# Optimization experiments

Hardware: AMD Instinct MI355X
Metric: run time of the kernel (lower is better)

Reference implementation:

```python
import jax, jax.numpy as jnp
import numpy as np

BATCH = 2048
TEMP = 0.5
EPS = 1e-12  # matches F.normalize default eps


def setup_inputs() -> dict:
    key = jax.random.key(0)
    k1, k2 = jax.random.split(key)
    emb_i = jax.random.normal(k1, (BATCH, 256), dtype=jnp.float32)
    emb_j = jax.random.normal(k2, (BATCH, 256), dtype=jnp.float32)
    return {"emb_i": emb_i, "emb_j": emb_j}


def _l2_normalize(x):
    norm = jnp.sqrt(jnp.sum(x * x, axis=1, keepdims=True))
    return x / jnp.maximum(norm, EPS)


def reference(emb_i, emb_j):
    n = emb_i.shape[0]  # = BATCH
    z_i = _l2_normalize(emb_i)
    z_j = _l2_normalize(emb_j)
    z = jnp.concatenate([z_i, z_j], axis=0)            # [2N, D]
    # cosine similarity of normalized vectors == plain GEMM
    sim = jnp.einsum('id,jd->ij', z, z)                # [2N, 2N]
    # positive pairs: diag offsets +N and -N
    sim_i_j = jnp.diagonal(sim, offset=n)              # [N]
    sim_j_i = jnp.diagonal(sim, offset=-n)             # [N]
    positives = jnp.concatenate([sim_i_j, sim_j_i])    # [2N]
    neg_mask = 1.0 - jnp.eye(2 * n, dtype=sim.dtype)   # [2N, 2N]
    numerator = jnp.exp(positives / TEMP)
    denominator = jnp.sum(neg_mask * jnp.exp(sim / TEMP), axis=1)  # [2N]
    loss_partial = -jnp.log(numerator / denominator)
    return jnp.sum(loss_partial) / (2 * n)
```

## Files before the change

### kernel.cpp

```cpp
#include <hip/hip_runtime.h>
#include <hip/hip_bf16.h>
#include <math.h>

#define NB        2048
#define TWO_N     4096
#define DIM       256
#define EPS       1e-12f
#define NT1D      (TWO_N / 128)
#define NTILES    (NT1D * (NT1D + 1) / 2)


typedef __attribute__((ext_vector_type(8))) short  bf16x8;
typedef __attribute__((ext_vector_type(4))) float  f32x4;

__global__ __launch_bounds__(256) void nrm_kernel(
    const float* __restrict__ emb_i, const float* __restrict__ emb_j,
    short* __restrict__ zt, float* __restrict__ pos,
    float* __restrict__ out)
{
    int t = threadIdx.x;
    int wave = t >> 6, lane = t & 63;
    int r = blockIdx.x * 4 + wave;
    float4 a = ((const float4*)(emb_i + (size_t)r * DIM))[lane];
    float4 b = ((const float4*)(emb_j + (size_t)r * DIM))[lane];
    float sa = a.x*a.x + a.y*a.y + a.z*a.z + a.w*a.w;
    float sb = b.x*b.x + b.y*b.y + b.z*b.z + b.w*b.w;
    float sd = a.x*b.x + a.y*b.y + a.z*b.z + a.w*b.w;
    #pragma unroll
    for (int off = 32; off >= 1; off >>= 1) {
        sa += __shfl_xor(sa, off, 64);
        sb += __shfl_xor(sb, off, 64);
        sd += __shfl_xor(sd, off, 64);
    }
    float si = 1.0f / fmaxf(sqrtf(sa), EPS);
    float sj = 1.0f / fmaxf(sqrtf(sb), EPS);

    int dst = (r >> 4) * 4096 + (lane >> 3) * 512 + ((lane >> 1) & 3) * 128
            + (r & 15) * 8 + (lane & 1) * 4;

    union { __hip_bfloat16 h[4]; uint2 u; } pk;
    pk.h[0] = __float2bfloat16(a.x * si);
    pk.h[1] = __float2bfloat16(a.y * si);
    pk.h[2] = __float2bfloat16(a.z * si);
    pk.h[3] = __float2bfloat16(a.w * si);
    *(uint2*)(zt + dst) = pk.u;
    pk.h[0] = __float2bfloat16(b.x * sj);
    pk.h[1] = __float2bfloat16(b.y * sj);
    pk.h[2] = __float2bfloat16(b.z * sj);
    pk.h[3] = __float2bfloat16(b.w * sj);
    *(uint2*)(zt + dst + 128 * 4096) = pk.u;

    if (lane == 0) pos[r] = sd * si * sj;
    if (blockIdx.x == 0 && t == 0) out[0] = 0.0f;
}

#define MFMA1(Av, Bv, m, n) \
    acc[m][n] = __builtin_amdgcn_mfma_f32_16x16x32_bf16(Av, Bv, acc[m][n], 0, 0, 0);

#define MFMA_ROW(Av, B0v, B1v, B2v, B3v, m) \
    MFMA1(Av, B0v, m, 0) MFMA1(Av, B1v, m, 1) \
    MFMA1(Av, B2v, m, 2) MFMA1(Av, B3v, m, 3)

#define MMSTEP(A0v, A1v, A2v, A3v, B0v, B1v, B2v, B3v) \
    MFMA_ROW(A0v, B0v, B1v, B2v, B3v, 0) \
    MFMA_ROW(A1v, B0v, B1v, B2v, B3v, 1) \
    MFMA_ROW(A2v, B0v, B1v, B2v, B3v, 2) \
    MFMA_ROW(A3v, B0v, B1v, B2v, B3v, 3)

#define SB __builtin_amdgcn_sched_barrier(0);

#define BAR \
    SB \
    asm volatile("s_waitcnt lgkmcnt(0)" ::: "memory"); \
    SB \
    __builtin_amdgcn_s_barrier(); \
    SB

#define SLDX(X, c) \
    G##X##0 = *(const bf16x8*)(stg_base + 0 * 4096 + (c) * 512); \
    G##X##1 = *(const bf16x8*)(stg_base + 1 * 4096 + (c) * 512); \
    G##X##2 = *(const bf16x8*)(stg_base + 2 * 4096 + (c) * 512); \
    G##X##3 = *(const bf16x8*)(stg_base + 3 * 4096 + (c) * 512);

#define DSWX(X, bs) \
    *(bf16x8*)&lds[(bs)*8192 + (p0+0)*512 + l8] = G##X##0; \
    *(bf16x8*)&lds[(bs)*8192 + (p0+1)*512 + l8] = G##X##1; \
    *(bf16x8*)&lds[(bs)*8192 + (p0+2)*512 + l8] = G##X##2; \
    *(bf16x8*)&lds[(bs)*8192 + (p0+3)*512 + l8] = G##X##3;

#define COMPUTE(bs) \
    { \
        bf16x8 fa0 = *(const bf16x8*)&lds[(bs)*8192 + (wm4+0)*512 + l8]; \
        bf16x8 fa1 = *(const bf16x8*)&lds[(bs)*8192 + (wm4+1)*512 + l8]; \
        bf16x8 fa2 = *(const bf16x8*)&lds[(bs)*8192 + (wm4+2)*512 + l8]; \
        bf16x8 fa3 = *(const bf16x8*)&lds[(bs)*8192 + (wm4+3)*512 + l8]; \
        bf16x8 fb0 = *(const bf16x8*)&lds[(bs)*8192 + 4096 + (wn4+0)*512 + l8]; \
        bf16x8 fb1 = *(const bf16x8*)&lds[(bs)*8192 + 4096 + (wn4+1)*512 + l8]; \
        bf16x8 fb2 = *(const bf16x8*)&lds[(bs)*8192 + 4096 + (wn4+2)*512 + l8]; \
        bf16x8 fb3 = *(const bf16x8*)&lds[(bs)*8192 + 4096 + (wn4+3)*512 + l8]; \
        MMSTEP(fa0, fa1, fa2, fa3, fb0, fb1, fb2, fb3) \
    }

__global__ __launch_bounds__(256, 3) void simexp_kernel(
    const short* __restrict__ zt, float* __restrict__ part)
{
    __shared__ short lds[2 * 8192];

    int id = blockIdx.x;
    int by = (int)((sqrtf(8.0f * (float)id + 1.0f) - 1.0f) * 0.5f);
    while ((by + 1) * (by + 2) / 2 <= id) ++by;
    while (by * (by + 1) / 2 > id) --by;
    int bx = id - by * (by + 1) / 2;

    int t = threadIdx.x;
    int w = t >> 6, lane = t & 63;
    int quad = lane >> 4, c16 = lane & 15;
    int wm = w >> 1, wn = w & 1;
    int wm4 = wm * 4, wn4 = wn * 4;
    int l8 = lane * 8;
    int p0 = w * 4;
    int rbase = bx * 128 + wm * 64;
    int jbase = by * 128 + wn * 64;

    const short* stg_base = zt
        + (size_t)((w < 2 ? bx : by) * 8 + (w & 1) * 4) * 4096 + l8;

    f32x4 acc[4][4];
    #pragma unroll
    for (int mt = 0; mt < 4; ++mt)
        #pragma unroll
        for (int nt = 0; nt < 4; ++nt)
            acc[mt][nt] = (f32x4){0.f, 0.f, 0.f, 0.f};

    bf16x8 GA0, GA1, GA2, GA3;
    bf16x8 GB0, GB1, GB2, GB3;

    SLDX(A, 0)
    DSWX(A, 0)
    SLDX(B, 1)
    BAR
    SLDX(A, 2) SB
    COMPUTE(0) SB
    DSWX(B, 1)
    BAR
    DSWX(A, 0) SB
    SLDX(B, 3) SB
    COMPUTE(1)
    BAR
    DSWX(B, 1) SB
    SLDX(A, 4) SB
    COMPUTE(0)
    BAR
    DSWX(A, 0) SB
    SLDX(B, 5) SB
    COMPUTE(1)
    BAR
    DSWX(B, 1) SB
    SLDX(A, 6) SB
    COMPUTE(0)
    BAR
    DSWX(A, 0) SB
    SLDX(B, 7) SB
    COMPUTE(1)
    BAR
    DSWX(B, 1) SB
    COMPUTE(0)
    BAR
    COMPUTE(1)

    float rsum[4][4];
    #pragma unroll
    for (int mt = 0; mt < 4; ++mt)
        #pragma unroll
        for (int rg = 0; rg < 4; ++rg) rsum[mt][rg] = 0.f;

    if (bx == by) {
        #pragma unroll
        for (int mt = 0; mt < 4; ++mt) {
            #pragma unroll
            for (int nt = 0; nt < 4; ++nt) {
                int j = jbase + nt * 16 + c16;
                #pragma unroll
                for (int rg = 0; rg < 4; ++rg) {
                    int r = rbase + mt * 16 + quad * 4 + rg;
                    float e = __expf(2.0f * acc[mt][nt][rg]);
                    rsum[mt][rg] += (r == j) ? 0.f : e;
                }
            }
        }
    } else {
        float csum[4] = {0.f, 0.f, 0.f, 0.f};
        #pragma unroll
        for (int mt = 0; mt < 4; ++mt) {
            #pragma unroll
            for (int nt = 0; nt < 4; ++nt) {
                #pragma unroll
                for (int rg = 0; rg < 4; ++rg) {
                    float e = __expf(2.0f * acc[mt][nt][rg]);
                    rsum[mt][rg] += e;
                    csum[nt] += e;
                }
            }
        }
        #pragma unroll
        for (int nt = 0; nt < 4; ++nt) {
            float v = csum[nt];
            v += __shfl_xor(v, 16, 64);
            v += __shfl_xor(v, 32, 64);
            if (quad == 0)
                part[(size_t)(by * 128 + wn * 64 + nt * 16 + c16) * 64
                     + 2 * bx + wm] = v;
        }
    }

    #pragma unroll
    for (int mt = 0; mt < 4; ++mt) {
        #pragma unroll
        for (int rg = 0; rg < 4; ++rg) {
            float v = rsum[mt][rg];
            v += __shfl_xor(v, 1, 64);
            v += __shfl_xor(v, 2, 64);
            v += __shfl_xor(v, 4, 64);
            v += __shfl_xor(v, 8, 64);
            if (c16 == 0)
                part[(size_t)(rbase + mt * 16 + quad * 4 + rg) * 64
                     + 2 * by + wn] = v;
        }
    }
}

__global__ __launch_bounds__(128) void redloss_kernel(
    const float* __restrict__ part, const float* __restrict__ pos,
    float* __restrict__ out)
{
    int s = blockIdx.x, t = threadIdx.x;
    int r = s * 128 + t;
    const float4* p = (const float4*)(part + ((size_t)r << 6));
    float sum = 0.f;
    #pragma unroll
    for (int i = 0; i < 16; ++i) {
        float4 v = p[i];
        sum += v.x + v.y + v.z + v.w;
    }
    float val = logf(sum) - 2.0f * pos[r & (NB - 1)];
    #pragma unroll
    for (int off = 32; off >= 1; off >>= 1) val += __shfl_xor(val, off, 64);
    __shared__ float red[2];
    if ((t & 63) == 0) red[t >> 6] = val;
    __syncthreads();
    if (t == 0)
        atomicAdd(out, (red[0] + red[1]) * (1.0f / (float)TWO_N));
}

extern "C" void kernel_launch(void* const* d_in, const int* in_sizes, int n_in,
                              void* d_out, int out_size, void* d_ws, size_t ws_size,
                              hipStream_t stream)
{
    const float* emb_i = (const float*)d_in[0];
    const float* emb_j = (const float*)d_in[1];
    float* out = (float*)d_out;

    short* zt = (short*)d_ws;
    float* part = (float*)((char*)d_ws + (size_t)TWO_N * DIM * sizeof(short));
    float* pos = part + (size_t)TWO_N * 64;

    nrm_kernel<<<NB / 4, 256, 0, stream>>>(emb_i, emb_j, zt, pos, out);
    simexp_kernel<<<NTILES, 256, 0, stream>>>(zt, part);
    redloss_kernel<<<NT1D, 128, 0, stream>>>(part, pos, out);
}
```

Before: 74.44 us.

## Stage GEMM tiles via direct global-to-LDS loads with triple buffering

Replaces the register-staged global loads plus LDS stores with global_load_lds, which writes straight into shared memory, and grows the LDS ring from two to three buffers. Loads for stage k+2 are issued while stage k computes, gated by explicit vmcnt waits. This is meant to save VGPRs and ds_write instructions and to hide more load latency, at the cost of 50% more LDS per block, which may affect occupancy. It also depends on the lane-to-address mapping of the direct-to-LDS loads matching the previous layout.

```diff
diff --git a/kernel.cpp b/kernel.cpp
--- a/kernel.cpp
+++ b/kernel.cpp
@@ -69,24 +69,23 @@
 
 #define SB __builtin_amdgcn_sched_barrier(0);
 
+#define WAITV(n) \
+    SB asm volatile("s_waitcnt vmcnt(" #n ")" ::: "memory"); SB
+
 #define BAR \
-    SB \
-    asm volatile("s_waitcnt lgkmcnt(0)" ::: "memory"); \
-    SB \
-    __builtin_amdgcn_s_barrier(); \
-    SB
-
-#define SLDX(X, c) \
-    G##X##0 = *(const bf16x8*)(stg_base + 0 * 4096 + (c) * 512); \
-    G##X##1 = *(const bf16x8*)(stg_base + 1 * 4096 + (c) * 512); \
-    G##X##2 = *(const bf16x8*)(stg_base + 2 * 4096 + (c) * 512); \
-    G##X##3 = *(const bf16x8*)(stg_base + 3 * 4096 + (c) * 512);
-
-#define DSWX(X, bs) \
-    *(bf16x8*)&lds[(bs)*8192 + (p0+0)*512 + l8] = G##X##0; \
-    *(bf16x8*)&lds[(bs)*8192 + (p0+1)*512 + l8] = G##X##1; \
-    *(bf16x8*)&lds[(bs)*8192 + (p0+2)*512 + l8] = G##X##2; \
-    *(bf16x8*)&lds[(bs)*8192 + (p0+3)*512 + l8] = G##X##3;
+    SB asm volatile("s_waitcnt lgkmcnt(0)" ::: "memory"); SB \
+    __builtin_amdgcn_s_barrier(); SB
+
+#define GLOAD(gsrc, ldst) \
+    __builtin_amdgcn_global_load_lds( \
+        (const __attribute__((address_space(1))) void*)(gsrc), \
+        (__attribute__((address_space(3))) void*)(ldst), 16, 0, 0);
+
+#define STAGE(c, bs) \
+    GLOAD(stg_base + 0 * 4096 + (c) * 512, &lds[(bs)*8192 + (p0+0)*512]) \
+    GLOAD(stg_base + 1 * 4096 + (c) * 512, &lds[(bs)*8192 + (p0+1)*512]) \
+    GLOAD(stg_base + 2 * 4096 + (c) * 512, &lds[(bs)*8192 + (p0+2)*512]) \
+    GLOAD(stg_base + 3 * 4096 + (c) * 512, &lds[(bs)*8192 + (p0+3)*512])
 
 #define COMPUTE(bs) \
     { \
@@ -104,7 +103,7 @@
 __global__ __launch_bounds__(256, 3) void simexp_kernel(
     const short* __restrict__ zt, float* __restrict__ part)
 {
-    __shared__ short lds[2 * 8192];
+    __shared__ short lds[3 * 8192];
 
     int id = blockIdx.x;
     int by = (int)((sqrtf(8.0f * (float)id + 1.0f) - 1.0f) * 0.5f);
@@ -132,39 +131,36 @@
         for (int nt = 0; nt < 4; ++nt)
             acc[mt][nt] = (f32x4){0.f, 0.f, 0.f, 0.f};
 
-    bf16x8 GA0, GA1, GA2, GA3;
-    bf16x8 GB0, GB1, GB2, GB3;
-
-    SLDX(A, 0)
-    DSWX(A, 0)
-    SLDX(B, 1)
-    BAR
-    SLDX(A, 2) SB
-    COMPUTE(0) SB
-    DSWX(B, 1)
-    BAR
-    DSWX(A, 0) SB
-    SLDX(B, 3) SB
+    STAGE(0, 0)
+    STAGE(1, 1)
+    WAITV(4)
+    BAR
+    STAGE(2, 2)
+    COMPUTE(0)
+    WAITV(4)
+    BAR
+    STAGE(3, 0)
     COMPUTE(1)
-    BAR
-    DSWX(B, 1) SB
-    SLDX(A, 4) SB
+    WAITV(4)
+    BAR
+    STAGE(4, 1)
+    COMPUTE(2)
+    WAITV(4)
+    BAR
+    STAGE(5, 2)
     COMPUTE(0)
-    BAR
-    DSWX(A, 0) SB
-    SLDX(B, 5) SB
+    WAITV(4)
+    BAR
+    STAGE(6, 0)
     COMPUTE(1)
-    BAR
-    DSWX(B, 1) SB
-    SLDX(A, 6) SB
+    WAITV(4)
+    BAR
+    STAGE(7, 1)
+    COMPUTE(2)
+    WAITV(4)
+    BAR
     COMPUTE(0)
-    BAR
-    DSWX(A, 0) SB
-    SLDX(B, 7) SB
-    COMPUTE(1)
-    BAR
-    DSWX(B, 1) SB
-    COMPUTE(0)
+    WAITV(0)
     BAR
     COMPUTE(1)
 
```

Result: no change. 73.75 us (-0.9%).
